# Performance work log

Measured on AMD Instinct MI355X. Metric: run time of the kernel, lower is better.

## Reference

```python
import jax, jax.numpy as jnp
import numpy as np

DIM, HEADS, KV_HEADS = 1024, 16, 4
B, T = 1, 4096
HEAD_DIM = DIM // HEADS           # 64
KV_DIM = DIM // (HEADS // KV_HEADS)  # 256
SCALE = HEAD_DIM ** -0.5


def setup_inputs() -> dict:
    key = jax.random.key(0)
    ks = jax.random.split(key, 9)
    s = lambda fan_in: fan_in ** -0.5
    return {
        "x": jax.random.normal(ks[0], (B, T, DIM), jnp.float32),
        "mask": jnp.tril(jnp.ones((1, 1, T, T), jnp.bool_)),  # causal
        "q_w": jax.random.normal(ks[1], (DIM, DIM), jnp.float32) * s(DIM),
        "q_b": jnp.zeros((DIM,), jnp.float32),
        "k_w": jax.random.normal(ks[2], (KV_DIM, DIM), jnp.float32) * s(DIM),
        "k_b": jnp.zeros((KV_DIM,), jnp.float32),
        "v_w": jax.random.normal(ks[3], (KV_DIM, DIM), jnp.float32) * s(DIM),
        "v_b": jnp.zeros((KV_DIM,), jnp.float32),
        "o_w": jax.random.normal(ks[4], (DIM, DIM), jnp.float32) * s(DIM),
        "o_b": jnp.zeros((DIM,), jnp.float32),
    }


def reference(x, mask, q_w, q_b, k_w, k_b, v_w, v_b, o_w, o_b):
    b, t, d = x.shape
    g = HEADS // KV_HEADS  # query heads per kv head
    # projections (torch Linear: x @ W^T + b)
    q = (x @ q_w.T + q_b).reshape(b, t, HEADS, HEAD_DIM).transpose(0, 2, 1, 3)      # [B,H,T,hd]
    k = (x @ k_w.T + k_b).reshape(b, t, KV_HEADS, HEAD_DIM).transpose(0, 2, 1, 3)   # [B,Hk,T,hd]
    v = (x @ v_w.T + v_b).reshape(b, t, KV_HEADS, HEAD_DIM).transpose(0, 2, 1, 3)   # [B,Hk,T,hd]
    # GQA: group query heads over shared kv heads
    qg = q.reshape(b, KV_HEADS, g, t, HEAD_DIM)                                     # [B,Hk,g,T,hd]
    scores = jnp.einsum('bkgtd,bksd->bkgts', qg, k) * SCALE                         # [B,Hk,g,T,T]
    scores = jnp.where(mask[:, :, None, :, :], scores, -1e9)
    attn = jax.nn.softmax(scores, axis=-1)  # dropout is identity in eval mode
    out = jnp.einsum('bkgts,bksd->bkgtd', attn, v)                                  # [B,Hk,g,T,hd]
    out = out.reshape(b, HEADS, t, HEAD_DIM).transpose(0, 2, 1, 3).reshape(b, t, d)
    out = out @ o_w.T + o_b
    return out, k, v  # (output, new kv cache)
```

## Files before the change

### kernel.cpp

```cpp
#include <hip/hip_runtime.h>
#include <hip/hip_bf16.h>
#include <stdint.h>

typedef __bf16 bf16;
typedef __bf16 bf16x8 __attribute__((ext_vector_type(8)));
typedef float  f32x4 __attribute__((ext_vector_type(4)));

#define SEQ   4096
#define DIM_  1024
#define HD_   64
#define NEG_BIG (-30000.0f)

__device__ __forceinline__ bf16x8 cvt8(const float* p) {
    f32x4 a = *(const f32x4*)p, b = *(const f32x4*)(p + 4);
    bf16x8 r;
    r[0]=(bf16)a[0]; r[1]=(bf16)a[1]; r[2]=(bf16)a[2]; r[3]=(bf16)a[3];
    r[4]=(bf16)b[0]; r[5]=(bf16)b[1]; r[6]=(bf16)b[2]; r[7]=(bf16)b[3];
    return r;
}

template<int MODE>
__global__ __launch_bounds__(256)
void gemm_bt(const void* __restrict__ Av,
             const float* __restrict__ B0, const float* __restrict__ b0,
             const float* __restrict__ B1, const float* __restrict__ b1,
             const float* __restrict__ B2, const float* __restrict__ b2,
             float* __restrict__ C0, float* __restrict__ C1, float* __restrict__ C2,
             bf16* __restrict__ Qbf, bf16* __restrict__ Kbf, bf16* __restrict__ VTbf)
{
    const int K = 1024;
    const int tid  = threadIdx.x;
    const int lane = tid & 63, wave = tid >> 6;
    const int qd = lane >> 4, ln = lane & 15;
    const int wm = (wave & 1) * 32, wn = (wave >> 1) * 64;
    const int m0 = blockIdx.x * 64, n0 = blockIdx.y * 128;

    const float* Bp; const float* bias;
    if (MODE == 1) {
        if (n0 < 1024)      { Bp = B0 + (size_t)n0 * K;        bias = b0 + n0; }
        else if (n0 < 1280) { Bp = B1 + (size_t)(n0-1024) * K; bias = b1 + (n0-1024); }
        else                { Bp = B2 + (size_t)(n0-1280) * K; bias = b2 + (n0-1280); }
    } else                  { Bp = B0 + (size_t)n0 * K;        bias = b0 + n0; }

    __shared__ bf16 As[64*32];
    __shared__ bf16 Bs[128*32];

    f32x4 acc[2][4] = {};

    for (int k0 = 0; k0 < K; k0 += 32) {
        bf16x8 ra, rb[2];
        {
            int row = tid >> 2, ch = tid & 3;
            if (MODE == 0)
                ra = *(const bf16x8*)((const bf16*)Av + (size_t)(m0+row)*K + k0 + ch*8);
            else
                ra = cvt8((const float*)Av + (size_t)(m0+row)*K + k0 + ch*8);
        }
        #pragma unroll
        for (int i = 0; i < 2; ++i) {
            int s = i*256 + tid;
            int row = s >> 2, ch = s & 3;
            rb[i] = cvt8(Bp + (size_t)row*K + k0 + ch*8);
        }
        __syncthreads();
        {
            int row = tid >> 2, ch = tid & 3;
            *(bf16x8*)(As + row*32 + ch*8) = ra;
        }
        #pragma unroll
        for (int i = 0; i < 2; ++i) {
            int s = i*256 + tid;
            int row = s >> 2, ch = s & 3;
            *(bf16x8*)(Bs + row*32 + ch*8) = rb[i];
        }
        __syncthreads();

        bf16x8 af[2], bg[4];
        #pragma unroll
        for (int i = 0; i < 2; ++i)
            af[i] = *(const bf16x8*)(As + (wm + i*16 + ln)*32 + qd*8);
        #pragma unroll
        for (int j = 0; j < 4; ++j)
            bg[j] = *(const bf16x8*)(Bs + (wn + j*16 + ln)*32 + qd*8);

        #pragma unroll
        for (int i = 0; i < 2; ++i)
            #pragma unroll
            for (int j = 0; j < 4; ++j)
                acc[i][j] = __builtin_amdgcn_mfma_f32_16x16x32_bf16(af[i], bg[j], acc[i][j], 0, 0, 0);
    }

    #pragma unroll
    for (int i = 0; i < 2; ++i) {
        #pragma unroll
        for (int j = 0; j < 4; ++j) {
            int colg = n0 + wn + j*16 + ln;
            float bv = bias[wn + j*16 + ln];
            #pragma unroll
            for (int r = 0; r < 4; ++r) {
                int rowg = m0 + wm + i*16 + qd*4 + r;
                float v = acc[i][j][r] + bv;
                if (MODE == 0) {
                    C0[(size_t)rowg*1024 + colg] = v;
                } else if (colg < 1024) {
                    Qbf[(size_t)rowg*1024 + colg] = (bf16)(v * 0.125f);
                } else if (colg < 1280) {
                    int c2 = colg - 1024;
                    size_t idx = (size_t)(c2 >> 6)*(SEQ*HD_) + (size_t)rowg*HD_ + (c2 & 63);
                    C1[idx]  = v;
                    Kbf[idx] = (bf16)v;
                } else {
                    int c2 = colg - 1280;
                    C2[(size_t)(c2 >> 6)*(SEQ*HD_) + (size_t)rowg*HD_ + (c2 & 63)] = v;
                    VTbf[(size_t)(c2 >> 6)*(HD_*SEQ) + (size_t)(c2 & 63)*SEQ + rowg] = (bf16)v;
                }
            }
        }
    }
}

__global__ __launch_bounds__(256)
void attn_fwd(const bf16* __restrict__ Q, const bf16* __restrict__ Kc,
              const bf16* __restrict__ VT, bf16* __restrict__ att)
{
    const int bid  = blockIdx.x;
    const int head = bid & 15;
    const int mt   = 63 - (bid >> 4);
    const int qb   = mt * 64;
    const int kvh  = head >> 2;

    const int tid = threadIdx.x, lane = tid & 63, wave = tid >> 6;
    const int qd = lane >> 4, ln = lane & 15;
    const int rw0 = qb + wave * 16;

    __shared__ bf16 Ks[64*72];
    __shared__ bf16 Vt[64*72];
    __shared__ bf16 Ps[4][16*72];

    const bf16* Kbase = Kc + (size_t)kvh * SEQ * HD_;
    const bf16* Vbase = VT + (size_t)kvh * HD_ * SEQ;

    bf16x8 aq[2];
    #pragma unroll
    for (int ks = 0; ks < 2; ++ks)
        aq[ks] = *(const bf16x8*)(Q + (size_t)(rw0 + ln)*DIM_ + head*HD_ + ks*32 + qd*8);

    f32x4 o[4] = {};
    float l_p[4] = {0.f, 0.f, 0.f, 0.f};

    const float LOG2E = 1.4426950408889634f;
    const float C16   = 16.0f * LOG2E;
    const int nkt = mt + 1;

    for (int kt = 0; kt < nkt; ++kt) {
        const int kb = kt * 64;

        bf16x8 rk[2], rv[2];
        #pragma unroll
        for (int i = 0; i < 2; ++i) {
            int s = i*256 + tid;
            int r8 = s >> 3, ch = s & 7;
            rk[i] = *(const bf16x8*)(Kbase + (size_t)(kb + r8)*HD_ + ch*8);
            rv[i] = *(const bf16x8*)(Vbase + (size_t)r8*SEQ + kb + ch*8);
        }
        __syncthreads();
        #pragma unroll
        for (int i = 0; i < 2; ++i) {
            int s = i*256 + tid;
            int r8 = s >> 3, ch = s & 7;
            *(bf16x8*)(Ks + r8*72 + ch*8) = rk[i];
            *(bf16x8*)(Vt + r8*72 + ch*8) = rv[i];
        }
        __syncthreads();

        f32x4 S[4] = {};
        #pragma unroll
        for (int ks = 0; ks < 2; ++ks) {
            bf16x8 bk[4];
            #pragma unroll
            for (int nf = 0; nf < 4; ++nf)
                bk[nf] = *(const bf16x8*)(Ks + (nf*16 + ln)*72 + ks*32 + qd*8);
            #pragma unroll
            for (int nf = 0; nf < 4; ++nf)
                S[nf] = __builtin_amdgcn_mfma_f32_16x16x32_bf16(aq[ks], bk[nf], S[nf], 0, 0, 0);
        }

        if (kt == nkt - 1) {
            #pragma unroll
            for (int nf = 0; nf < 4; ++nf) {
                int col = kb + nf*16 + ln;
                #pragma unroll
                for (int r = 0; r < 4; ++r) {
                    int row = rw0 + qd*4 + r;
                    if (col > row) S[nf][r] = NEG_BIG;
                }
            }
        }

        bf16* Pw = &Ps[wave][0];
        #pragma unroll
        for (int r = 0; r < 4; ++r) {
            #pragma unroll
            for (int nf = 0; nf < 4; ++nf) {
                float p = exp2f(S[nf][r] * LOG2E - C16);
                l_p[r] += p;
                Pw[(qd*4 + r)*72 + nf*16 + ln] = (bf16)p;
            }
        }
        asm volatile("s_waitcnt lgkmcnt(0)" ::: "memory");

        #pragma unroll
        for (int ks = 0; ks < 2; ++ks) {
            bf16x8 bv[4];
            #pragma unroll
            for (int nf = 0; nf < 4; ++nf)
                bv[nf] = *(const bf16x8*)(Vt + (nf*16 + ln)*72 + ks*32 + qd*8);
            bf16x8 ap = *(const bf16x8*)(&Ps[wave][ln*72 + ks*32 + qd*8]);
            #pragma unroll
            for (int nf = 0; nf < 4; ++nf)
                o[nf] = __builtin_amdgcn_mfma_f32_16x16x32_bf16(ap, bv[nf], o[nf], 0, 0, 0);
        }
    }

    #pragma unroll
    for (int r = 0; r < 4; ++r) {
        float l = l_p[r];
        l += __shfl_xor(l, 1);
        l += __shfl_xor(l, 2);
        l += __shfl_xor(l, 4);
        l += __shfl_xor(l, 8);
        float inv = 1.0f / l;
        int trow = rw0 + qd*4 + r;
        #pragma unroll
        for (int nf = 0; nf < 4; ++nf)
            att[(size_t)trow*DIM_ + head*HD_ + nf*16 + ln] = (bf16)(o[nf][r] * inv);
    }
}

extern "C" void kernel_launch(void* const* d_in, const int* in_sizes, int n_in,
                              void* d_out, int out_size, void* d_ws, size_t ws_size,
                              hipStream_t stream)
{
    const float* x  = (const float*)d_in[0];
    const float* qw = (const float*)d_in[2];
    const float* qb = (const float*)d_in[3];
    const float* kw = (const float*)d_in[4];
    const float* kb = (const float*)d_in[5];
    const float* vw = (const float*)d_in[6];
    const float* vb = (const float*)d_in[7];
    const float* ow = (const float*)d_in[8];
    const float* ob = (const float*)d_in[9];

    float* out  = (float*)d_out;
    float* kout = out  + (size_t)SEQ * DIM_;
    float* vout = kout + (size_t)4 * SEQ * HD_;

    bf16* q_bf  = (bf16*)d_out;
    bf16* k_bf  = q_bf + (size_t)SEQ * DIM_;
    bf16* vT_bf = k_bf + (size_t)4 * SEQ * HD_;
    bf16* att   = (bf16*)d_ws;

    gemm_bt<1><<<dim3(64, 12), 256, 0, stream>>>(x, qw, qb, kw, kb, vw, vb,
                                                 nullptr, kout, vout,
                                                 q_bf, k_bf, vT_bf);
    attn_fwd<<<dim3(1024), 256, 0, stream>>>(q_bf, k_bf, vT_bf, att);
    gemm_bt<0><<<dim3(64, 8), 256, 0, stream>>>(att, ow, ob, nullptr, nullptr,
                                                nullptr, nullptr, out, nullptr, nullptr,
                                                nullptr, nullptr, nullptr);
}
```

Baseline: 265.2 us.

## Pre-convert inputs and weights to bf16 and load GEMM tiles via direct-to-LDS loads

Adds a conversion kernel that writes x and all projection weights as bf16 into scratch space in the output and workspace buffers. The GEMMs then fetch tiles with global_load_lds straight into shared memory, instead of loading fp32, converting in registers and storing to LDS. This removes the repeated fp32 reads and conversions that happen across the tile grid, at the cost of an extra kernel launch and an extra pass over the inputs. The o_w conversion is used only if the workspace is large enough; otherwise the old fp32 path remains.

```diff
diff --git a/kernel.cpp b/kernel.cpp
--- a/kernel.cpp
+++ b/kernel.cpp
@@ -19,12 +19,37 @@
     return r;
 }
 
-template<int MODE>
+__device__ __forceinline__ void gload16(const bf16* g, bf16* l) {
+    __builtin_amdgcn_global_load_lds(
+        (const __attribute__((address_space(1))) void*)g,
+        (__attribute__((address_space(3))) void*)l, 16, 0, 0);
+}
+
 __global__ __launch_bounds__(256)
-void gemm_bt(const void* __restrict__ Av,
-             const float* __restrict__ B0, const float* __restrict__ b0,
-             const float* __restrict__ B1, const float* __restrict__ b1,
-             const float* __restrict__ B2, const float* __restrict__ b2,
+void conv_bf16(const float* __restrict__ x,  const float* __restrict__ qw,
+               const float* __restrict__ kw, const float* __restrict__ vw,
+               const float* __restrict__ ow,
+               bf16* __restrict__ xb,  bf16* __restrict__ qwb,
+               bf16* __restrict__ kwb, bf16* __restrict__ vwb,
+               bf16* __restrict__ owb)
+{
+    int b = blockIdx.x;
+    const float* s; bf16* d; int base;
+    if (b < 2048)      { s = x;  d = xb;  base = b * 2048; }
+    else if (b < 2560) { s = qw; d = qwb; base = (b - 2048) * 2048; }
+    else if (b < 2688) { s = kw; d = kwb; base = (b - 2560) * 2048; }
+    else if (b < 2816) { s = vw; d = vwb; base = (b - 2688) * 2048; }
+    else               { s = ow; d = owb; base = (b - 2816) * 2048; }
+    int i = base + threadIdx.x * 8;
+    *(bf16x8*)(d + i) = cvt8(s + i);
+}
+
+template<int MODE, bool BWBF>
+__global__ __launch_bounds__(256)
+void gemm_bt(const bf16* __restrict__ A,
+             const void* __restrict__ B0, const float* __restrict__ b0,
+             const void* __restrict__ B1, const float* __restrict__ b1,
+             const void* __restrict__ B2, const float* __restrict__ b2,
              float* __restrict__ C0, float* __restrict__ C1, float* __restrict__ C2,
              bf16* __restrict__ Qbf, bf16* __restrict__ Kbf, bf16* __restrict__ VTbf)
 {
@@ -35,45 +60,52 @@
     const int wm = (wave & 1) * 32, wn = (wave >> 1) * 64;
     const int m0 = blockIdx.x * 64, n0 = blockIdx.y * 128;
 
-    const float* Bp; const float* bias;
+    const void* Bp; const float* bias;
     if (MODE == 1) {
-        if (n0 < 1024)      { Bp = B0 + (size_t)n0 * K;        bias = b0 + n0; }
-        else if (n0 < 1280) { Bp = B1 + (size_t)(n0-1024) * K; bias = b1 + (n0-1024); }
-        else                { Bp = B2 + (size_t)(n0-1280) * K; bias = b2 + (n0-1280); }
-    } else                  { Bp = B0 + (size_t)n0 * K;        bias = b0 + n0; }
+        if (n0 < 1024)      { Bp = (const bf16*)B0 + (size_t)n0 * K;        bias = b0 + n0; }
+        else if (n0 < 1280) { Bp = (const bf16*)B1 + (size_t)(n0-1024) * K; bias = b1 + (n0-1024); }
+        else                { Bp = (const bf16*)B2 + (size_t)(n0-1280) * K; bias = b2 + (n0-1280); }
+    } else if (BWBF)        { Bp = (const bf16*)B0 + (size_t)n0 * K;        bias = b0 + n0; }
+    else                    { Bp = (const float*)B0 + (size_t)n0 * K;       bias = b0 + n0; }
 
     __shared__ bf16 As[64*32];
     __shared__ bf16 Bs[128*32];
 
+    const int gr = lane >> 2, gc = (lane & 3) * 8;
+    const bf16* Ag  = A + (size_t)(m0 + wave*16 + gr) * K + gc;
+    bf16* AsW = As + wave*16*32;
+    const bf16* Bg0 = (const bf16*)Bp + (size_t)(wave*32 + gr) * K + gc;
+    const bf16* Bg1 = (const bf16*)Bp + (size_t)(wave*32 + 16 + gr) * K + gc;
+    bf16* BsW0 = Bs + (wave*32) * 32;
+    bf16* BsW1 = Bs + (wave*32 + 16) * 32;
+
     f32x4 acc[2][4] = {};
 
     for (int k0 = 0; k0 < K; k0 += 32) {
-        bf16x8 ra, rb[2];
-        {
-            int row = tid >> 2, ch = tid & 3;
-            if (MODE == 0)
-                ra = *(const bf16x8*)((const bf16*)Av + (size_t)(m0+row)*K + k0 + ch*8);
-            else
-                ra = cvt8((const float*)Av + (size_t)(m0+row)*K + k0 + ch*8);
-        }
-        #pragma unroll
-        for (int i = 0; i < 2; ++i) {
-            int s = i*256 + tid;
-            int row = s >> 2, ch = s & 3;
-            rb[i] = cvt8(Bp + (size_t)row*K + k0 + ch*8);
-        }
-        __syncthreads();
-        {
-            int row = tid >> 2, ch = tid & 3;
-            *(bf16x8*)(As + row*32 + ch*8) = ra;
-        }
-        #pragma unroll
-        for (int i = 0; i < 2; ++i) {
-            int s = i*256 + tid;
-            int row = s >> 2, ch = s & 3;
-            *(bf16x8*)(Bs + row*32 + ch*8) = rb[i];
-        }
-        __syncthreads();
+        if constexpr (MODE == 1 || BWBF) {
+            __syncthreads();
+            gload16(Ag  + k0, AsW);
+            gload16(Bg0 + k0, BsW0);
+            gload16(Bg1 + k0, BsW1);
+            __syncthreads();
+        } else {
+            bf16x8 rb[2];
+            #pragma unroll
+            for (int i = 0; i < 2; ++i) {
+                int s = i*256 + tid;
+                int row = s >> 2, ch = s & 3;
+                rb[i] = cvt8((const float*)Bp + (size_t)row*K + k0 + ch*8);
+            }
+            __syncthreads();
+            gload16(Ag + k0, AsW);
+            #pragma unroll
+            for (int i = 0; i < 2; ++i) {
+                int s = i*256 + tid;
+                int row = s >> 2, ch = s & 3;
+                *(bf16x8*)(Bs + row*32 + ch*8) = rb[i];
+            }
+            __syncthreads();
+        }
 
         bf16x8 af[2], bg[4];
         #pragma unroll
@@ -256,15 +288,31 @@
     float* vout = kout + (size_t)4 * SEQ * HD_;
 
     bf16* q_bf  = (bf16*)d_out;
-    bf16* k_bf  = q_bf + (size_t)SEQ * DIM_;
-    bf16* vT_bf = k_bf + (size_t)4 * SEQ * HD_;
-    bf16* att   = (bf16*)d_ws;
-
-    gemm_bt<1><<<dim3(64, 12), 256, 0, stream>>>(x, qw, qb, kw, kb, vw, vb,
-                                                 nullptr, kout, vout,
-                                                 q_bf, k_bf, vT_bf);
+    bf16* k_bf  = q_bf  + (size_t)SEQ * DIM_;
+    bf16* vT_bf = k_bf  + (size_t)4 * SEQ * HD_;
+    bf16* qw_bf = vT_bf + (size_t)4 * HD_ * SEQ;
+    bf16* kw_bf = qw_bf + (size_t)1024 * 1024;
+    bf16* vw_bf = kw_bf + (size_t)256 * 1024;
+
+    bf16* x_bf = (bf16*)d_ws;
+    bf16* att  = (bf16*)d_ws;
+    bool  owbf_ok = ws_size >= (size_t)(8*1024*1024 + 2*1024*1024);
+    bf16* ow_bf = owbf_ok ? (bf16*)((char*)d_ws + (size_t)8*1024*1024) : nullptr;
+
+    int convBlocks = 2816 + (owbf_ok ? 512 : 0);
+    conv_bf16<<<convBlocks, 256, 0, stream>>>(x, qw, kw, vw, ow,
+                                              x_bf, qw_bf, kw_bf, vw_bf, ow_bf);
+
+    gemm_bt<1, true><<<dim3(64, 12), 256, 0, stream>>>(x_bf, qw_bf, qb, kw_bf, kb, vw_bf, vb,
+                                                       nullptr, kout, vout,
+                                                       q_bf, k_bf, vT_bf);
     attn_fwd<<<dim3(1024), 256, 0, stream>>>(q_bf, k_bf, vT_bf, att);
-    gemm_bt<0><<<dim3(64, 8), 256, 0, stream>>>(att, ow, ob, nullptr, nullptr,
-                                                nullptr, nullptr, out, nullptr, nullptr,
-                                                nullptr, nullptr, nullptr);
-}
+    if (owbf_ok)
+        gemm_bt<0, true><<<dim3(64, 8), 256, 0, stream>>>(att, ow_bf, ob, nullptr, nullptr,
+                                                          nullptr, nullptr, out, nullptr, nullptr,
+                                                          nullptr, nullptr, nullptr);
+    else
+        gemm_bt<0, false><<<dim3(64, 8), 256, 0, stream>>>(att, ow, ob, nullptr, nullptr,
+                                                           nullptr, nullptr, out, nullptr, nullptr,
+                                                           nullptr, nullptr, nullptr);
+}
```

After: 254.6 us. -4.0%, faster.
